# Optimization experiments

Hardware: AMD Instinct MI355X
Metric: run time of the kernel (lower is better)

Reference implementation:

```python
import jax, jax.numpy as jnp
import numpy as np

H = 1024; W = 1024
SPACE_SIGMA = 16.0; RANGE_SIGMA = 0.25
PAD_XY = 2; PAD_Z = 2
DIM = 5


def setup_inputs() -> dict:
    key = jax.random.key(0)
    k1, k2 = jax.random.split(key)
    features = jax.random.uniform(k1, (H, W, 3), dtype=jnp.float32)
    inp = jax.random.normal(k2, (H, W, 3), dtype=jnp.float32)
    return {"features": features, "inp": inp}


def _grid_dims(features_np):
    # Grid sizes are data-dependent in the original (TF builds them from
    # per-channel min/max); compute them host-side from concrete inputs.
    sh = int(float(H - 1) / SPACE_SIGMA) + 1 + 2 * PAD_XY
    sw = int(float(W - 1) / SPACE_SIGMA) + 1 + 2 * PAD_XY
    depths = []
    for c in range(3):
        ch = features_np[..., c]
        delta = float(ch.max() - ch.min())
        depths.append(int(delta / RANGE_SIGMA) + 1 + 2 * PAD_Z)
    return (sh, sw, depths[0], depths[1], depths[2])


def _both_indices(size, coord):
    left = jnp.clip(coord.astype(jnp.int32), 0, size - 1)
    right = jnp.clip(left + 1, 0, size - 1)
    return left, right


def _convn(data, n_iter=2):
    # Faithful port of the TF convn: separable [1,2,1]/4 pass per axis with
    # the exact same ping-pong buffer / boundary-keep / transpose behavior.
    buffer = jnp.zeros_like(data)
    perm = (1, 2, 3, 4, 0)
    for _ in range(n_iter):
        buffer, data = data, buffer
        for _ in range(DIM):
            newdata = (buffer[:-2] + buffer[2:] + 2.0 * buffer[1:-1]) / 4.0
            data = jnp.concatenate([data[:1], newdata, data[-1:]], axis=0)
            data = jnp.transpose(data, perm)
            buffer = jnp.transpose(buffer, perm)
    return data


def _filter(features, inp, dims):
    sh, sw, dr, dg, db = dims
    hw = H * W
    yy, xx = jnp.meshgrid(jnp.arange(H, dtype=jnp.float32),
                          jnp.arange(W, dtype=jnp.float32), indexing="ij")
    splat_yy = (yy / SPACE_SIGMA + 0.5).astype(jnp.int32) + PAD_XY
    splat_xx = (xx / SPACE_SIGMA + 0.5).astype(jnp.int32) + PAD_XY
    slice_yy = yy / SPACE_SIGMA + PAD_XY
    slice_xx = xx / SPACE_SIGMA + PAD_XY
    y_i, y_i2 = _both_indices(sh, slice_yy)
    x_i, x_i2 = _both_indices(sw, slice_xx)
    y_alpha = (slice_yy - y_i.astype(jnp.float32)).reshape(-1)
    x_alpha = (slice_xx - x_i.astype(jnp.float32)).reshape(-1)

    chans = []
    for c, depth in zip(range(3), (dr, dg, db)):
        v = features[..., c]
        v0 = v - jnp.min(v)
        splat_v = (v0 / RANGE_SIGMA + 0.5).astype(jnp.int32) + PAD_Z
        slice_v = v0 / RANGE_SIGMA + PAD_Z
        li, ri = _both_indices(depth, slice_v)
        alpha = (slice_v - li.astype(jnp.float32)).reshape(-1)
        chans.append((splat_v, li, ri, alpha))
    (splat_rr, r_i, r_i2, r_alpha) = chans[0]
    (splat_gg, g_i, g_i2, g_alpha) = chans[1]
    (splat_bb, b_i, b_i2, b_alpha) = chans[2]

    splat_coords = ((((splat_yy * sw + splat_xx) * dr + splat_rr) * dg
                     + splat_gg) * db + splat_bb).reshape(-1)  # [hw]

    idx_all = jnp.stack([y_i, y_i2, x_i, x_i2, r_i, r_i2,
                         g_i, g_i2, b_i, b_i2]).reshape(10, hw)
    alphas_all = jnp.stack([1.0 - y_alpha, y_alpha, 1.0 - x_alpha, x_alpha,
                            1.0 - r_alpha, r_alpha, 1.0 - g_alpha, g_alpha,
                            1.0 - b_alpha, b_alpha])  # [10, hw]

    # 32 corners of the 5-D hypercube; sel[c, d] picks left/right index per dim.
    corners = np.stack(np.meshgrid(*([np.arange(2)] * DIM), indexing="ij"),
                       axis=-1).reshape(-1, DIM)
    sel = corners + np.arange(DIM) * 2  # [32, 5]

    strides = (sw, dr, dg, db)
    coord = idx_all[sel[:, 0]]  # [32, hw]
    for d in range(1, DIM):
        coord = coord * strides[d - 1] + idx_all[sel[:, d]]
    alpha_prod = alphas_all[sel[:, 0]]  # [32, hw]
    for d in range(1, DIM):
        alpha_prod = alpha_prod * alphas_all[sel[:, d]]

    total = sh * sw * dr * dg * db

    def ch_filter(ch):
        grid = jnp.zeros((total,), jnp.float32).at[splat_coords].add(ch.reshape(-1))
        grid = _convn(grid.reshape(sh, sw, dr, dg, db))
        vals = grid.reshape(-1)[coord]  # [32, hw] multilinear gather
        return jnp.sum(alpha_prod * vals, axis=0).reshape(H, W)

    outT = jax.vmap(ch_filter)(jnp.transpose(inp, (2, 0, 1)))
    return jnp.transpose(outT, (1, 2, 0))


def reference(features, inp):
    dims = _grid_dims(np.asarray(features))
    return _filter(features, inp, dims)
```

## Files before the change

kernel.cpp:

```cpp
#include <hip/hip_runtime.h>

namespace {

constexpr int kH  = 1024;
constexpr int kW  = 1024;
constexpr int kHW = kH * kW;
constexpr int kSH = 68;
constexpr int kSW = 68;
constexpr int kD  = 8;
constexpr int kT3 = kSH * kSW * kD * kD * kD;

__global__ void minmax_kernel(const float* __restrict__ feat, float* __restrict__ part) {
    const float4* f4 = (const float4*)feat;
    float mn[3] = {1e30f, 1e30f, 1e30f};
    float mx[3] = {-1e30f, -1e30f, -1e30f};
    int tid = blockIdx.x * blockDim.x + threadIdx.x;
    int stride = gridDim.x * blockDim.x;
    for (int c = tid; c < kHW / 4; c += stride) {
        float4 q0 = f4[c * 3], q1 = f4[c * 3 + 1], q2 = f4[c * 3 + 2];
        mn[0] = fminf(mn[0], fminf(fminf(q0.x, q0.w), fminf(q1.z, q2.y)));
        mx[0] = fmaxf(mx[0], fmaxf(fmaxf(q0.x, q0.w), fmaxf(q1.z, q2.y)));
        mn[1] = fminf(mn[1], fminf(fminf(q0.y, q1.x), fminf(q1.w, q2.z)));
        mx[1] = fmaxf(mx[1], fmaxf(fmaxf(q0.y, q1.x), fmaxf(q1.w, q2.z)));
        mn[2] = fminf(mn[2], fminf(fminf(q0.z, q1.y), fminf(q2.x, q2.w)));
        mx[2] = fmaxf(mx[2], fmaxf(fmaxf(q0.z, q1.y), fmaxf(q2.x, q2.w)));
    }
    #pragma unroll
    for (int off = 32; off > 0; off >>= 1) {
        #pragma unroll
        for (int c = 0; c < 3; ++c) {
            mn[c] = fminf(mn[c], __shfl_down(mn[c], off, 64));
            mx[c] = fmaxf(mx[c], __shfl_down(mx[c], off, 64));
        }
    }
    __shared__ float smn[4][3], smx[4][3];
    int wave = threadIdx.x >> 6;
    if ((threadIdx.x & 63) == 0) {
        #pragma unroll
        for (int c = 0; c < 3; ++c) { smn[wave][c] = mn[c]; smx[wave][c] = mx[c]; }
    }
    __syncthreads();
    if (threadIdx.x == 0) {
        #pragma unroll
        for (int c = 0; c < 3; ++c) {
            part[blockIdx.x * 6 + c]     = fminf(fminf(smn[0][c], smn[1][c]), fminf(smn[2][c], smn[3][c]));
            part[blockIdx.x * 6 + 3 + c] = fmaxf(fmaxf(smx[0][c], smx[1][c]), fmaxf(smx[2][c], smx[3][c]));
        }
    }
}

__global__ void params_kernel(const float* __restrict__ part, float* __restrict__ hdrF) {
    int t = threadIdx.x;
    float mn[3], mx[3];
    #pragma unroll
    for (int c = 0; c < 3; ++c) { mn[c] = part[t * 6 + c]; mx[c] = part[t * 6 + 3 + c]; }
    #pragma unroll
    for (int off = 32; off > 0; off >>= 1) {
        #pragma unroll
        for (int c = 0; c < 3; ++c) {
            mn[c] = fminf(mn[c], __shfl_down(mn[c], off, 64));
            mx[c] = fmaxf(mx[c], __shfl_down(mx[c], off, 64));
        }
    }
    __shared__ float smn[4][3], smx[4][3];
    int wave = t >> 6;
    if ((t & 63) == 0) {
        #pragma unroll
        for (int c = 0; c < 3; ++c) { smn[wave][c] = mn[c]; smx[wave][c] = mx[c]; }
    }
    __syncthreads();
    if (t == 0) {
        int* ip = (int*)(hdrF + 8);
        #pragma unroll
        for (int c = 0; c < 3; ++c) {
            float bmn = fminf(fminf(smn[0][c], smn[1][c]), fminf(smn[2][c], smn[3][c]));
            float bmx = fmaxf(fmaxf(smx[0][c], smx[1][c]), fmaxf(smx[2][c], smx[3][c]));
            float delta = bmx - bmn;
            int depth = (int)((double)delta / 0.25) + 1 + 4;
            if (depth > kD) depth = kD;
            if (depth < 1) depth = 1;
            hdrF[c] = bmn;
            ip[c] = depth;
        }
    }
}

__global__ __launch_bounds__(256) void splat_kernel(const float* __restrict__ feat,
                                                    const float* __restrict__ inp,
                                                    const float* __restrict__ hdrF,
                                                    float* __restrict__ grid) {
    int ix = blockIdx.x, iy = blockIdx.y;
    int y0 = (iy == 0) ? 0 : 16 * iy - 8;
    int x0 = (ix == 0) ? 0 : 16 * ix - 8;
    int h = (iy == 0 || iy == 64) ? 8 : 16;
    int w = (ix == 0 || ix == 64) ? 8 : 16;

    __shared__ float acc[3 * 512];
    __shared__ float fS[16 * 48], iS[16 * 48];
    for (int i = threadIdx.x; i < 3 * 512; i += 256) acc[i] = 0.0f;

    int rowVec = (w * 3) >> 2;
    int nvec = h * rowVec;
    const float4* f4 = (const float4*)(feat + ((long)y0 * kW + x0) * 3);
    const float4* i4 = (const float4*)(inp  + ((long)y0 * kW + x0) * 3);
    for (int t = threadIdx.x; t < nvec; t += 256) {
        int row = t / rowVec, q = t - row * rowVec;
        ((float4*)fS)[row * rowVec + q] = f4[row * (kW * 3 / 4) + q];
        ((float4*)iS)[row * rowVec + q] = i4[row * (kW * 3 / 4) + q];
    }
    __syncthreads();

    int t = threadIdx.x;
    int n = w * h;
    if (t < n) {
        int lx = t & (w - 1);
        int ly = (w == 16) ? (t >> 4) : (t >> 3);
        int o = (ly * w + lx) * 3;
        float v0 = fS[o + 0] - hdrF[0];
        float v1 = fS[o + 1] - hdrF[1];
        float v2 = fS[o + 2] - hdrF[2];
        int sr = (int)(v0 * 4.0f + 0.5f) + 2;
        int sg = (int)(v1 * 4.0f + 0.5f) + 2;
        int sb = (int)(v2 * 4.0f + 0.5f) + 2;
        int ci = (sr << 6) + (sg << 3) + sb;
        atomicAdd(&acc[ci],        iS[o + 0]);
        atomicAdd(&acc[512 + ci],  iS[o + 1]);
        atomicAdd(&acc[1024 + ci], iS[o + 2]);
    }
    __syncthreads();

    long base = ((long)((iy + 2) * kSW + (ix + 2))) << 9;
    for (int i = threadIdx.x; i < 512; i += 256) {
        int b = i >> 6, r = (i >> 3) & 7, g = i & 7;
        int s = (r << 6) + (g << 3) + b;
        grid[base + i]            = acc[s];
        grid[kT3 + base + i]      = acc[512 + s];
        grid[2 * kT3 + base + i]  = acc[1024 + s];
    }
}

__global__ __launch_bounds__(192) void blur2_kernel(float* __restrict__ dst,
                                                    const float* __restrict__ src,
                                                    const float* __restrict__ hdrF) {
    int cx = blockIdx.x + 2, cy = blockIdx.y + 2;
    const int* ip = (const int*)(hdrF + 8);
    int dr = ip[0], dg = ip[1], db = ip[2];

    __shared__ float Sv[3 * 576];
    long cbase = ((long)(cy * kSW + cx)) << 9;

    {
        const float4* g4 = (const float4*)src;
        for (int i = threadIdx.x; i < 384; i += 192) {
            int ch = i >> 7, i4 = i & 127;
            float4 q = g4[(long)ch * (kT3 / 4) + (cbase >> 2) + i4];
            int b = i4 >> 4;
            int rg = ((i4 >> 1) & 7) * 8 + (i4 & 1) * 4;
            *(float4*)&Sv[ch * 576 + b * 72 + rg] = q;
        }
    }
    __syncthreads();

    int ch = threadIdx.x >> 6;
    int rg = threadIdx.x & 63;
    int r = rg >> 3, g = rg & 7;

    float* S = Sv + ch * 576;
    auto SV = [&](int b, int l) -> float { return S[b * 72 + l]; };
    auto gsp = [&](int ccy, int ccx, int rr, int gg, int bb) -> float {
        if (ccy < 2 || ccy > 66 || ccx < 2 || ccx > 66) return 0.0f;
        return src[(long)ch * kT3 + (((long)(ccy * kSW + ccx)) << 9) + (bb << 6) + (rr << 3) + gg];
    };

    bool gI = (g >= 1) && (g <= dg - 2);
    bool rI = (r >= 1) && (r <= dr - 2);

    float v[8];
    #pragma unroll
    for (int b = 0; b < 8; ++b) v[b] = SV(b, rg);

    int eHi = db - 1;

    auto o1_end = [&](int e) -> float {
        float Vm, Vp;
        if (gI)      { Vm = SV(e, rg - 1); Vp = SV(e, rg + 1); }
        else if (rI) { Vm = SV(e, rg - 8); Vp = SV(e, rg + 8); }
        else         { Vm = gsp(cy, cx - 1, r, g, e); Vp = gsp(cy, cx + 1, r, g, e); }
        return (Vm + Vp + 2.0f * SV(e, rg)) * 0.25f;
    };
    float o1_lo = o1_end(0);
    float o1_hi = o1_end(eHi);

    float o1[8];
    #pragma unroll
    for (int b = 0; b < 8; ++b) {
        float iv = 0.0f;
        if (b >= 1 && b <= 6) iv = ((v[b - 1] + v[b + 1]) + 2.0f * v[b]) * 0.25f;
        o1[b] = (b >= 1 && b <= db - 2) ? iv : (b == 0 ? o1_lo : (b == eHi ? o1_hi : 0.0f));
    }

    auto out1_in = [&](int r2, int g2, int e) -> float {
        int l2 = (r2 << 3) + g2;
        float C = SV(e, l2);
        float Nm, Np;
        if (g2 >= 1 && g2 <= dg - 2)      { Nm = SV(e, l2 - 1); Np = SV(e, l2 + 1); }
        else if (r2 >= 1 && r2 <= dr - 2) { Nm = SV(e, l2 - 8); Np = SV(e, l2 + 8); }
        else { Nm = gsp(cy, cx - 1, r2, g2, e); Np = gsp(cy, cx + 1, r2, g2, e); }
        return (Nm + Np + 2.0f * C) * 0.25f;
    };
    auto out1_x = [&](int cx2, int e) -> float {
        float C = gsp(cy, cx2, r, g, e);
        float Nm, Np;
        if (cx2 >= 1 && cx2 <= kSW - 2) { Nm = gsp(cy, cx2 - 1, r, g, e); Np = gsp(cy, cx2 + 1, r, g, e); }
        else                            { Nm = gsp(cy - 1, cx2, r, g, e); Np = gsp(cy + 1, cx2, r, g, e); }
        return (Nm + Np + 2.0f * C) * 0.25f;
    };
    auto o2_end = [&](int e, float o1e) -> float {
        float Xm, Xp;
        if (gI)      { Xm = out1_in(r, g - 1, e); Xp = out1_in(r, g + 1, e); }
        else if (rI) { Xm = out1_in(r - 1, g, e); Xp = out1_in(r + 1, g, e); }
        else         { Xm = out1_x(cx - 1, e);    Xp = out1_x(cx + 1, e); }
        return (Xm + Xp + 2.0f * o1e) * 0.25f;
    };
    float o2_lo = o2_end(0, o1_lo);
    float o2_hi = o2_end(eHi, o1_hi);

    float o2[8];
    #pragma unroll
    for (int b = 0; b < 8; ++b) {
        float iv = 0.0f;
        if (b >= 1 && b <= 6) iv = ((o1[b - 1] + o1[b + 1]) + 2.0f * o1[b]) * 0.25f;
        o2[b] = (b >= 1 && b <= db - 2) ? iv : (b == 0 ? o2_lo : (b == eHi ? o2_hi : 0.0f));
    }

    float* dp = dst + (long)ch * kT3 + cbase + (rg << 3);
    *(float4*)dp       = make_float4(o2[0], o2[1], o2[2], o2[3]);
    *(float4*)(dp + 4) = make_float4(o2[4], o2[5], o2[6], o2[7]);
}

__global__ __launch_bounds__(256) void slice_kernel(const float* __restrict__ feat,
                                                    const float* __restrict__ hdrF,
                                                    const float* __restrict__ grid,
                                                    float* __restrict__ out) {
    __shared__ float sg[3 * 4 * 512 + 8];
    int tx = blockIdx.x, ty = blockIdx.y;

    {
        const float4* g4 = (const float4*)grid;
        float4* s4 = (float4*)sg;
        #pragma unroll
        for (int it = 0; it < 2; ++it) {
            int i = threadIdx.x + it * 256;
            int cell = i >> 7;
            int ci4 = i & 127;
            int cy = ty + 2 + (cell >> 1), cx = tx + 2 + (cell & 1);
            long cbase4 = ((long)(cy * kSW + cx)) << 7;
            #pragma unroll
            for (int ch = 0; ch < 3; ++ch)
                s4[ch * 512 + i] = g4[(long)ch * (kT3 / 4) + cbase4 + ci4];
        }
    }
    __syncthreads();

    const int* ip = (const int*)(hdrF + 8);
    int d3[3] = {ip[0], ip[1], ip[2]};
    int lx = threadIdx.x & 15, ly = threadIdx.x >> 4;
    int y = (ty << 4) + ly, x = (tx << 4) + lx;
    int p = (y << 10) + x;

    float ya = (float)ly * 0.0625f;
    float xa = (float)lx * 0.0625f;

    int li[3], ri[3];
    float al[3];
    #pragma unroll
    for (int c = 0; c < 3; ++c) {
        float v0 = feat[p * 3 + c] - hdrF[c];
        float sv = v0 * 4.0f + 2.0f;
        int l = (int)sv;
        int dm = d3[c] - 1;
        l = l < 0 ? 0 : (l > dm ? dm : l);
        int rr = l + 1 > dm ? dm : l + 1;
        li[c] = l; ri[c] = rr; al[c] = sv - (float)l;
    }

    float spw[4];
    {
        float wy[2] = {1.0f - ya, ya};
        float wx[2] = {1.0f - xa, xa};
        spw[0] = wy[0] * wx[0]; spw[1] = wy[0] * wx[1];
        spw[2] = wy[1] * wx[0]; spw[3] = wy[1] * wx[1];
    }
    int rs[2] = {li[0], ri[0]}; float wrr[2] = {1.0f - al[0], al[0]};
    int gs[2] = {li[1], ri[1]}; float wgg[2] = {1.0f - al[1], al[1]};
    int bq = li[2];
    float aeff = (ri[2] > li[2]) ? al[2] : 0.0f;

    float acc0 = 0.0f, acc1 = 0.0f, acc2 = 0.0f;
    #pragma unroll
    for (int k = 0; k < 4; ++k) {
        #pragma unroll
        for (int cr = 0; cr < 2; ++cr)
        #pragma unroll
        for (int cg = 0; cg < 2; ++cg) {
            int si = (k << 9) + (rs[cr] << 6) + (gs[cg] << 3) + bq;
            float w = spw[k] * wrr[cr] * wgg[cg];
            float a0 = sg[si],        a1 = sg[si + 1];
            float b0 = sg[2048 + si], b1 = sg[2048 + si + 1];
            float c0 = sg[4096 + si], c1 = sg[4096 + si + 1];
            acc0 += w * (a0 + aeff * (a1 - a0));
            acc1 += w * (b0 + aeff * (b1 - b0));
            acc2 += w * (c0 + aeff * (c1 - c0));
        }
    }
    out[p * 3 + 0] = acc0;
    out[p * 3 + 1] = acc1;
    out[p * 3 + 2] = acc2;
}

}

extern "C" void kernel_launch(void* const* d_in, const int* in_sizes, int n_in,
                              void* d_out, int out_size, void* d_ws, size_t ws_size,
                              hipStream_t stream) {
    const float* feat = (const float*)d_in[0];
    const float* inp  = (const float*)d_in[1];
    float* out = (float*)d_out;

    float* hdrF  = (float*)d_ws;
    float* part  = (float*)((char*)d_ws + 1024);
    float* gridA = (float*)((char*)d_ws + 8192);
    float* gridB = gridA + 3 * (size_t)kT3;

    minmax_kernel<<<256, 256, 0, stream>>>(feat, part);
    params_kernel<<<1, 256, 0, stream>>>(part, hdrF);

    splat_kernel<<<dim3(65, 65), 256, 0, stream>>>(feat, inp, hdrF, gridA);
    blur2_kernel<<<dim3(65, 65), 192, 0, stream>>>(gridB, gridA, hdrF);
    slice_kernel<<<dim3(64, 64), 256, 0, stream>>>(feat, hdrF, gridB, out);
}
```

Before: 142.2 us.

## Fuse all stages into one persistent cooperative kernel with grid syncs

Replaces the five separate launches (minmax, params, splat, blur, slice) with a single cooperative kernel of 512 persistent blocks that loops over cells and tiles, separating the stages with grid.sync(). The aim is to remove per-launch overhead and the gaps between kernels. In exchange, each stage runs with only 512 blocks instead of thousands, and the grid-wide barriers add cost. The original kernels are kept as a fallback if the cooperative launch fails.

```diff
diff --git a/kernel.cpp b/kernel.cpp
--- a/kernel.cpp
+++ b/kernel.cpp
@@ -1,19 +1,348 @@
 #include <hip/hip_runtime.h>
+#include <hip/hip_cooperative_groups.h>
+
+namespace cg = cooperative_groups;
+
+#define kH  1024
+#define kW  1024
+#define kHW (kH * kW)
+#define kSH 68
+#define kSW 68
+#define kD  8
+#define kT3 (kSH * kSW * kD * kD * kD)
+#define kNB 512
 
 namespace {
 
-constexpr int kH  = 1024;
-constexpr int kW  = 1024;
-constexpr int kHW = kH * kW;
-constexpr int kSH = 68;
-constexpr int kSW = 68;
-constexpr int kD  = 8;
-constexpr int kT3 = kSH * kSW * kD * kD * kD;
-
-__global__ void minmax_kernel(const float* __restrict__ feat, float* __restrict__ part) {
+__global__ __launch_bounds__(256, 2)
+void mega_kernel(const float* __restrict__ feat,
+                 const float* __restrict__ inp,
+                 float* __restrict__ out,
+                 float* __restrict__ hdrF,
+                 float* __restrict__ part,
+                 float* __restrict__ gridA,
+                 float* __restrict__ gridB) {
+    cg::grid_group grid = cg::this_grid();
+    __shared__ float S[6160];
+
+    {
+        const float4* f4 = (const float4*)feat;
+        float mn[3] = {1e30f, 1e30f, 1e30f}, mx[3] = {-1e30f, -1e30f, -1e30f};
+        for (int c = blockIdx.x * 256 + threadIdx.x; c < kHW / 4; c += kNB * 256) {
+            float4 q0 = f4[c * 3], q1 = f4[c * 3 + 1], q2 = f4[c * 3 + 2];
+            mn[0] = fminf(mn[0], fminf(fminf(q0.x, q0.w), fminf(q1.z, q2.y)));
+            mx[0] = fmaxf(mx[0], fmaxf(fmaxf(q0.x, q0.w), fmaxf(q1.z, q2.y)));
+            mn[1] = fminf(mn[1], fminf(fminf(q0.y, q1.x), fminf(q1.w, q2.z)));
+            mx[1] = fmaxf(mx[1], fmaxf(fmaxf(q0.y, q1.x), fmaxf(q1.w, q2.z)));
+            mn[2] = fminf(mn[2], fminf(fminf(q0.z, q1.y), fminf(q2.x, q2.w)));
+            mx[2] = fmaxf(mx[2], fmaxf(fmaxf(q0.z, q1.y), fmaxf(q2.x, q2.w)));
+        }
+        #pragma unroll
+        for (int off = 32; off > 0; off >>= 1) {
+            #pragma unroll
+            for (int k = 0; k < 3; ++k) {
+                mn[k] = fminf(mn[k], __shfl_down(mn[k], off, 64));
+                mx[k] = fmaxf(mx[k], __shfl_down(mx[k], off, 64));
+            }
+        }
+        int wave = threadIdx.x >> 6;
+        if ((threadIdx.x & 63) == 0) {
+            #pragma unroll
+            for (int k = 0; k < 3; ++k) { S[wave * 3 + k] = mn[k]; S[12 + wave * 3 + k] = mx[k]; }
+        }
+        __syncthreads();
+        if (threadIdx.x == 0) {
+            #pragma unroll
+            for (int k = 0; k < 3; ++k) {
+                part[blockIdx.x * 6 + k]     = fminf(fminf(S[k], S[3 + k]), fminf(S[6 + k], S[9 + k]));
+                part[blockIdx.x * 6 + 3 + k] = fmaxf(fmaxf(S[12 + k], S[15 + k]), fmaxf(S[18 + k], S[21 + k]));
+            }
+        }
+        __syncthreads();
+    }
+    grid.sync();
+
+    if (blockIdx.x == 0) {
+        int t = threadIdx.x;
+        float mn[3] = {1e30f, 1e30f, 1e30f}, mx[3] = {-1e30f, -1e30f, -1e30f};
+        #pragma unroll
+        for (int j = 0; j < 2; ++j) {
+            int idx = t + j * 256;
+            #pragma unroll
+            for (int k = 0; k < 3; ++k) {
+                mn[k] = fminf(mn[k], part[idx * 6 + k]);
+                mx[k] = fmaxf(mx[k], part[idx * 6 + 3 + k]);
+            }
+        }
+        #pragma unroll
+        for (int off = 32; off > 0; off >>= 1) {
+            #pragma unroll
+            for (int k = 0; k < 3; ++k) {
+                mn[k] = fminf(mn[k], __shfl_down(mn[k], off, 64));
+                mx[k] = fmaxf(mx[k], __shfl_down(mx[k], off, 64));
+            }
+        }
+        int wave = t >> 6;
+        if ((t & 63) == 0) {
+            #pragma unroll
+            for (int k = 0; k < 3; ++k) { S[wave * 3 + k] = mn[k]; S[12 + wave * 3 + k] = mx[k]; }
+        }
+        __syncthreads();
+        if (t == 0) {
+            int* ip = (int*)(hdrF + 8);
+            #pragma unroll
+            for (int k = 0; k < 3; ++k) {
+                float bmn = fminf(fminf(S[k], S[3 + k]), fminf(S[6 + k], S[9 + k]));
+                float bmx = fmaxf(fmaxf(S[12 + k], S[15 + k]), fmaxf(S[18 + k], S[21 + k]));
+                float delta = bmx - bmn;
+                int depth = (int)((double)delta / 0.25) + 1 + 4;
+                if (depth > kD) depth = kD;
+                if (depth < 1) depth = 1;
+                hdrF[k] = bmn;
+                ip[k] = depth;
+            }
+        }
+    }
+    grid.sync();
+
+    float m0 = hdrF[0], m1 = hdrF[1], m2 = hdrF[2];
+    const int* ip = (const int*)(hdrF + 8);
+    int dr = ip[0], dg = ip[1], db = ip[2];
+
+    {
+        float* acc = S;
+        float* fS  = S + 1536;
+        float* iS  = S + 2304;
+        for (int cell = blockIdx.x; cell < 65 * 65; cell += kNB) {
+            int iy = cell / 65, ix = cell % 65;
+            int y0 = (iy == 0) ? 0 : 16 * iy - 8;
+            int x0 = (ix == 0) ? 0 : 16 * ix - 8;
+            int h = (iy == 0 || iy == 64) ? 8 : 16;
+            int w = (ix == 0 || ix == 64) ? 8 : 16;
+
+            for (int i = threadIdx.x; i < 1536; i += 256) acc[i] = 0.0f;
+
+            int rowVec = (w * 3) >> 2;
+            int nvec = h * rowVec;
+            const float4* f4 = (const float4*)(feat + ((long)y0 * kW + x0) * 3);
+            const float4* i4 = (const float4*)(inp  + ((long)y0 * kW + x0) * 3);
+            for (int t = threadIdx.x; t < nvec; t += 256) {
+                int row = t / rowVec, q = t - row * rowVec;
+                ((float4*)fS)[row * rowVec + q] = f4[row * (kW * 3 / 4) + q];
+                ((float4*)iS)[row * rowVec + q] = i4[row * (kW * 3 / 4) + q];
+            }
+            __syncthreads();
+
+            int t = threadIdx.x;
+            if (t < w * h) {
+                int lx = t & (w - 1);
+                int ly = (w == 16) ? (t >> 4) : (t >> 3);
+                int o = (ly * w + lx) * 3;
+                int sr  = (int)((fS[o + 0] - m0) * 4.0f + 0.5f) + 2;
+                int sg2 = (int)((fS[o + 1] - m1) * 4.0f + 0.5f) + 2;
+                int sb  = (int)((fS[o + 2] - m2) * 4.0f + 0.5f) + 2;
+                int ci = (sr << 6) + (sg2 << 3) + sb;
+                atomicAdd(&acc[ci],        iS[o + 0]);
+                atomicAdd(&acc[512 + ci],  iS[o + 1]);
+                atomicAdd(&acc[1024 + ci], iS[o + 2]);
+            }
+            __syncthreads();
+
+            long base = ((long)((iy + 2) * kSW + (ix + 2))) << 9;
+            for (int i = threadIdx.x; i < 512; i += 256) {
+                int b = i >> 6, r = (i >> 3) & 7, g = i & 7;
+                int s = (r << 6) + (g << 3) + b;
+                gridA[base + i]            = acc[s];
+                gridA[kT3 + base + i]      = acc[512 + s];
+                gridA[2 * kT3 + base + i]  = acc[1024 + s];
+            }
+            __syncthreads();
+        }
+    }
+    grid.sync();
+
+    {
+        float* Sv = S;
+        for (int cell = blockIdx.x; cell < 65 * 65; cell += kNB) {
+            int cy = cell / 65 + 2, cx = cell % 65 + 2;
+            long cbase = ((long)(cy * kSW + cx)) << 9;
+            {
+                const float4* g4 = (const float4*)gridA;
+                for (int i = threadIdx.x; i < 384; i += 256) {
+                    int ch = i >> 7, i4 = i & 127;
+                    float4 q = g4[(long)ch * (kT3 / 4) + (cbase >> 2) + i4];
+                    int b = i4 >> 4;
+                    int rg = ((i4 >> 1) & 7) * 8 + (i4 & 1) * 4;
+                    *(float4*)&Sv[ch * 576 + b * 72 + rg] = q;
+                }
+            }
+            __syncthreads();
+
+            if (threadIdx.x < 192) {
+                int ch = threadIdx.x >> 6;
+                int rg = threadIdx.x & 63;
+                int r = rg >> 3, g = rg & 7;
+
+                float* Sc = Sv + ch * 576;
+                auto SV = [&](int b, int l) -> float { return Sc[b * 72 + l]; };
+                auto gsp = [&](int ccy, int ccx, int rr, int gg, int bb) -> float {
+                    if (ccy < 2 || ccy > 66 || ccx < 2 || ccx > 66) return 0.0f;
+                    return gridA[(long)ch * kT3 + (((long)(ccy * kSW + ccx)) << 9) + (bb << 6) + (rr << 3) + gg];
+                };
+
+                bool gI = (g >= 1) && (g <= dg - 2);
+                bool rI = (r >= 1) && (r <= dr - 2);
+
+                float v[8];
+                #pragma unroll
+                for (int b = 0; b < 8; ++b) v[b] = SV(b, rg);
+
+                int eHi = db - 1;
+
+                auto o1_end = [&](int e) -> float {
+                    float Vm, Vp;
+                    if (gI)      { Vm = SV(e, rg - 1); Vp = SV(e, rg + 1); }
+                    else if (rI) { Vm = SV(e, rg - 8); Vp = SV(e, rg + 8); }
+                    else         { Vm = gsp(cy, cx - 1, r, g, e); Vp = gsp(cy, cx + 1, r, g, e); }
+                    return (Vm + Vp + 2.0f * SV(e, rg)) * 0.25f;
+                };
+                float o1_lo = o1_end(0);
+                float o1_hi = o1_end(eHi);
+
+                float o1[8];
+                #pragma unroll
+                for (int b = 0; b < 8; ++b) {
+                    float iv = 0.0f;
+                    if (b >= 1 && b <= 6) iv = ((v[b - 1] + v[b + 1]) + 2.0f * v[b]) * 0.25f;
+                    o1[b] = (b >= 1 && b <= db - 2) ? iv : (b == 0 ? o1_lo : (b == eHi ? o1_hi : 0.0f));
+                }
+
+                auto out1_in = [&](int r2, int g2, int e) -> float {
+                    int l2 = (r2 << 3) + g2;
+                    float C = SV(e, l2);
+                    float Nm, Np;
+                    if (g2 >= 1 && g2 <= dg - 2)      { Nm = SV(e, l2 - 1); Np = SV(e, l2 + 1); }
+                    else if (r2 >= 1 && r2 <= dr - 2) { Nm = SV(e, l2 - 8); Np = SV(e, l2 + 8); }
+                    else { Nm = gsp(cy, cx - 1, r2, g2, e); Np = gsp(cy, cx + 1, r2, g2, e); }
+                    return (Nm + Np + 2.0f * C) * 0.25f;
+                };
+                auto out1_x = [&](int cx2, int e) -> float {
+                    float C = gsp(cy, cx2, r, g, e);
+                    float Nm, Np;
+                    if (cx2 >= 1 && cx2 <= kSW - 2) { Nm = gsp(cy, cx2 - 1, r, g, e); Np = gsp(cy, cx2 + 1, r, g, e); }
+                    else                            { Nm = gsp(cy - 1, cx2, r, g, e); Np = gsp(cy + 1, cx2, r, g, e); }
+                    return (Nm + Np + 2.0f * C) * 0.25f;
+                };
+                auto o2_end = [&](int e, float o1e) -> float {
+                    float Xm, Xp;
+                    if (gI)      { Xm = out1_in(r, g - 1, e); Xp = out1_in(r, g + 1, e); }
+                    else if (rI) { Xm = out1_in(r - 1, g, e); Xp = out1_in(r + 1, g, e); }
+                    else         { Xm = out1_x(cx - 1, e);    Xp = out1_x(cx + 1, e); }
+                    return (Xm + Xp + 2.0f * o1e) * 0.25f;
+                };
+                float o2_lo = o2_end(0, o1_lo);
+                float o2_hi = o2_end(eHi, o1_hi);
+
+                float o2[8];
+                #pragma unroll
+                for (int b = 0; b < 8; ++b) {
+                    float iv = 0.0f;
+                    if (b >= 1 && b <= 6) iv = ((o1[b - 1] + o1[b + 1]) + 2.0f * o1[b]) * 0.25f;
+                    o2[b] = (b >= 1 && b <= db - 2) ? iv : (b == 0 ? o2_lo : (b == eHi ? o2_hi : 0.0f));
+                }
+
+                float* dp = gridB + (long)ch * kT3 + cbase + (rg << 3);
+                *(float4*)dp       = make_float4(o2[0], o2[1], o2[2], o2[3]);
+                *(float4*)(dp + 4) = make_float4(o2[4], o2[5], o2[6], o2[7]);
+            }
+            __syncthreads();
+        }
+    }
+    grid.sync();
+
+    {
+        float* sg = S;
+        for (int tile = blockIdx.x; tile < 64 * 64; tile += kNB) {
+            int ty = tile >> 6, tx = tile & 63;
+            {
+                const float4* g4 = (const float4*)gridB;
+                float4* s4 = (float4*)sg;
+                #pragma unroll
+                for (int it = 0; it < 2; ++it) {
+                    int i = threadIdx.x + it * 256;
+                    int cell = i >> 7;
+                    int ci4 = i & 127;
+                    int cy = ty + 2 + (cell >> 1), cx = tx + 2 + (cell & 1);
+                    long cbase4 = ((long)(cy * kSW + cx)) << 7;
+                    #pragma unroll
+                    for (int ch = 0; ch < 3; ++ch)
+                        s4[ch * 512 + i] = g4[(long)ch * (kT3 / 4) + cbase4 + ci4];
+                }
+            }
+            __syncthreads();
+
+            int lx = threadIdx.x & 15, ly = threadIdx.x >> 4;
+            int y = (ty << 4) + ly, x = (tx << 4) + lx;
+            int p = (y << 10) + x;
+
+            float ya = (float)ly * 0.0625f;
+            float xa = (float)lx * 0.0625f;
+
+            int d3[3] = {dr, dg, db};
+            float mm[3] = {m0, m1, m2};
+            int li[3], ri[3];
+            float al[3];
+            #pragma unroll
+            for (int c = 0; c < 3; ++c) {
+                float v0 = feat[p * 3 + c] - mm[c];
+                float sv = v0 * 4.0f + 2.0f;
+                int l = (int)sv;
+                int dm = d3[c] - 1;
+                l = l < 0 ? 0 : (l > dm ? dm : l);
+                int rr = l + 1 > dm ? dm : l + 1;
+                li[c] = l; ri[c] = rr; al[c] = sv - (float)l;
+            }
+
+            float spw[4];
+            {
+                float wy[2] = {1.0f - ya, ya};
+                float wx[2] = {1.0f - xa, xa};
+                spw[0] = wy[0] * wx[0]; spw[1] = wy[0] * wx[1];
+                spw[2] = wy[1] * wx[0]; spw[3] = wy[1] * wx[1];
+            }
+            int rs[2] = {li[0], ri[0]}; float wrr[2] = {1.0f - al[0], al[0]};
+            int gs[2] = {li[1], ri[1]}; float wgg[2] = {1.0f - al[1], al[1]};
+            int bq = li[2];
+            float aeff = (ri[2] > li[2]) ? al[2] : 0.0f;
+
+            float acc0 = 0.0f, acc1 = 0.0f, acc2 = 0.0f;
+            #pragma unroll
+            for (int k = 0; k < 4; ++k) {
+                #pragma unroll
+                for (int cr = 0; cr < 2; ++cr)
+                #pragma unroll
+                for (int cg = 0; cg < 2; ++cg) {
+                    int si = (k << 9) + (rs[cr] << 6) + (gs[cg] << 3) + bq;
+                    float w = spw[k] * wrr[cr] * wgg[cg];
+                    float a0 = sg[si],        a1 = sg[si + 1];
+                    float b0 = sg[2048 + si], b1 = sg[2048 + si + 1];
+                    float c0 = sg[4096 + si], c1 = sg[4096 + si + 1];
+                    acc0 += w * (a0 + aeff * (a1 - a0));
+                    acc1 += w * (b0 + aeff * (b1 - b0));
+                    acc2 += w * (c0 + aeff * (c1 - c0));
+                }
+            }
+            out[p * 3 + 0] = acc0;
+            out[p * 3 + 1] = acc1;
+            out[p * 3 + 2] = acc2;
+            __syncthreads();
+        }
+    }
+}
+
+__global__ void fb_minmax(const float* __restrict__ feat, float* __restrict__ part) {
     const float4* f4 = (const float4*)feat;
-    float mn[3] = {1e30f, 1e30f, 1e30f};
-    float mx[3] = {-1e30f, -1e30f, -1e30f};
+    float mn[3] = {1e30f, 1e30f, 1e30f}, mx[3] = {-1e30f, -1e30f, -1e30f};
     int tid = blockIdx.x * blockDim.x + threadIdx.x;
     int stride = gridDim.x * blockDim.x;
     for (int c = tid; c < kHW / 4; c += stride) {
@@ -49,7 +378,7 @@
     }
 }
 
-__global__ void params_kernel(const float* __restrict__ part, float* __restrict__ hdrF) {
+__global__ void fb_params(const float* __restrict__ part, float* __restrict__ hdrF) {
     int t = threadIdx.x;
     float mn[3], mx[3];
     #pragma unroll
@@ -85,10 +414,10 @@
     }
 }
 
-__global__ __launch_bounds__(256) void splat_kernel(const float* __restrict__ feat,
-                                                    const float* __restrict__ inp,
-                                                    const float* __restrict__ hdrF,
-                                                    float* __restrict__ grid) {
+__global__ __launch_bounds__(256) void fb_splat(const float* __restrict__ feat,
+                                                const float* __restrict__ inp,
+                                                const float* __restrict__ hdrF,
+                                                float* __restrict__ grid) {
     int ix = blockIdx.x, iy = blockIdx.y;
     int y0 = (iy == 0) ? 0 : 16 * iy - 8;
     int x0 = (ix == 0) ? 0 : 16 * ix - 8;
@@ -111,17 +440,13 @@
     __syncthreads();
 
     int t = threadIdx.x;
-    int n = w * h;
-    if (t < n) {
+    if (t < w * h) {
         int lx = t & (w - 1);
         int ly = (w == 16) ? (t >> 4) : (t >> 3);
         int o = (ly * w + lx) * 3;
-        float v0 = fS[o + 0] - hdrF[0];
-        float v1 = fS[o + 1] - hdrF[1];
-        float v2 = fS[o + 2] - hdrF[2];
-        int sr = (int)(v0 * 4.0f + 0.5f) + 2;
-        int sg = (int)(v1 * 4.0f + 0.5f) + 2;
-        int sb = (int)(v2 * 4.0f + 0.5f) + 2;
+        int sr = (int)((fS[o + 0] - hdrF[0]) * 4.0f + 0.5f) + 2;
+        int sg = (int)((fS[o + 1] - hdrF[1]) * 4.0f + 0.5f) + 2;
+        int sb = (int)((fS[o + 2] - hdrF[2]) * 4.0f + 0.5f) + 2;
         int ci = (sr << 6) + (sg << 3) + sb;
         atomicAdd(&acc[ci],        iS[o + 0]);
         atomicAdd(&acc[512 + ci],  iS[o + 1]);
@@ -139,9 +464,9 @@
     }
 }
 
-__global__ __launch_bounds__(192) void blur2_kernel(float* __restrict__ dst,
-                                                    const float* __restrict__ src,
-                                                    const float* __restrict__ hdrF) {
+__global__ __launch_bounds__(192) void fb_blur2(float* __restrict__ dst,
+                                                const float* __restrict__ src,
+                                                const float* __restrict__ hdrF) {
     int cx = blockIdx.x + 2, cy = blockIdx.y + 2;
     const int* ip = (const int*)(hdrF + 8);
     int dr = ip[0], dg = ip[1], db = ip[2];
@@ -238,10 +563,10 @@
     *(float4*)(dp + 4) = make_float4(o2[4], o2[5], o2[6], o2[7]);
 }
 
-__global__ __launch_bounds__(256) void slice_kernel(const float* __restrict__ feat,
-                                                    const float* __restrict__ hdrF,
-                                                    const float* __restrict__ grid,
-                                                    float* __restrict__ out) {
+__global__ __launch_bounds__(256) void fb_slice(const float* __restrict__ feat,
+                                                const float* __restrict__ hdrF,
+                                                const float* __restrict__ grid,
+                                                float* __restrict__ out) {
     __shared__ float sg[3 * 4 * 512 + 8];
     int tx = blockIdx.x, ty = blockIdx.y;
 
@@ -328,14 +653,19 @@
     float* out = (float*)d_out;
 
     float* hdrF  = (float*)d_ws;
-    float* part  = (float*)((char*)d_ws + 1024);
-    float* gridA = (float*)((char*)d_ws + 8192);
+    float* part  = (float*)((char*)d_ws + 16384);
+    float* gridA = (float*)((char*)d_ws + 65536);
     float* gridB = gridA + 3 * (size_t)kT3;
 
-    minmax_kernel<<<256, 256, 0, stream>>>(feat, part);
-    params_kernel<<<1, 256, 0, stream>>>(part, hdrF);
-
-    splat_kernel<<<dim3(65, 65), 256, 0, stream>>>(feat, inp, hdrF, gridA);
-    blur2_kernel<<<dim3(65, 65), 192, 0, stream>>>(gridB, gridA, hdrF);
-    slice_kernel<<<dim3(64, 64), 256, 0, stream>>>(feat, hdrF, gridB, out);
-}
+    void* args[] = {(void*)&feat, (void*)&inp, (void*)&out,
+                    (void*)&hdrF, (void*)&part, (void*)&gridA, (void*)&gridB};
+    hipError_t err = hipLaunchCooperativeKernel((const void*)mega_kernel, dim3(kNB),
+                                                dim3(256), args, 0, stream);
+    if (err != hipSuccess) {
+        fb_minmax<<<256, 256, 0, stream>>>(feat, part);
+        fb_params<<<1, 256, 0, stream>>>(part, hdrF);
+        fb_splat<<<dim3(65, 65), 256, 0, stream>>>(feat, inp, hdrF, gridA);
+        fb_blur2<<<dim3(65, 65), 192, 0, stream>>>(gridB, gridA, hdrF);
+        fb_slice<<<dim3(64, 64), 256, 0, stream>>>(feat, hdrF, gridB, out);
+    }
+}
```

Measured after the change: 386.3 us. 2.72x slower.

## Store bilateral grids in fp16 and fold the params reduction into consumer kernels

Applied to the files above, without the earlier changes.

The intermediate splat and blurred grids are now stored as half precision, halving their memory footprint and traffic in splat, blur and slice, with conversion to float on load into shared memory. The single-block params kernel is removed. Each consumer block instead re-reduces the 256 per-block min/max partials itself, which drops one launch and its serialization but repeats a small reduction in every block. fp16 storage of accumulated grid sums adds rounding error and could overflow for large sums.

```diff
diff --git a/kernel.cpp b/kernel.cpp
--- a/kernel.cpp
+++ b/kernel.cpp
@@ -1,4 +1,5 @@
 #include <hip/hip_runtime.h>
+#include <hip/hip_fp16.h>
 
 namespace {
 
@@ -10,10 +11,51 @@
 constexpr int kD  = 8;
 constexpr int kT3 = kSH * kSW * kD * kD * kD;
 
+template <int NT>
+__device__ inline void load_params(const float* __restrict__ part,
+                                   float mOut[3], int dOut[3]) {
+    __shared__ float pm[NT / 64][6];
+    float mn[3] = {1e30f, 1e30f, 1e30f}, mx[3] = {-1e30f, -1e30f, -1e30f};
+    for (int idx = threadIdx.x; idx < 256; idx += NT) {
+        #pragma unroll
+        for (int c = 0; c < 3; ++c) {
+            mn[c] = fminf(mn[c], part[idx * 6 + c]);
+            mx[c] = fmaxf(mx[c], part[idx * 6 + 3 + c]);
+        }
+    }
+    #pragma unroll
+    for (int off = 32; off > 0; off >>= 1) {
+        #pragma unroll
+        for (int c = 0; c < 3; ++c) {
+            mn[c] = fminf(mn[c], __shfl_down(mn[c], off, 64));
+            mx[c] = fmaxf(mx[c], __shfl_down(mx[c], off, 64));
+        }
+    }
+    int wave = threadIdx.x >> 6;
+    if ((threadIdx.x & 63) == 0) {
+        #pragma unroll
+        for (int c = 0; c < 3; ++c) { pm[wave][c] = mn[c]; pm[wave][3 + c] = mx[c]; }
+    }
+    __syncthreads();
+    #pragma unroll
+    for (int c = 0; c < 3; ++c) {
+        float bmn = pm[0][c], bmx = pm[0][3 + c];
+        #pragma unroll
+        for (int w = 1; w < NT / 64; ++w) {
+            bmn = fminf(bmn, pm[w][c]);
+            bmx = fmaxf(bmx, pm[w][3 + c]);
+        }
+        float delta = bmx - bmn;
+        int depth = (int)((double)delta / 0.25) + 1 + 4;
+        depth = depth > kD ? kD : (depth < 1 ? 1 : depth);
+        mOut[c] = bmn;
+        dOut[c] = depth;
+    }
+}
+
 __global__ void minmax_kernel(const float* __restrict__ feat, float* __restrict__ part) {
     const float4* f4 = (const float4*)feat;
-    float mn[3] = {1e30f, 1e30f, 1e30f};
-    float mx[3] = {-1e30f, -1e30f, -1e30f};
+    float mn[3] = {1e30f, 1e30f, 1e30f}, mx[3] = {-1e30f, -1e30f, -1e30f};
     int tid = blockIdx.x * blockDim.x + threadIdx.x;
     int stride = gridDim.x * blockDim.x;
     for (int c = tid; c < kHW / 4; c += stride) {
@@ -49,46 +91,13 @@
     }
 }
 
-__global__ void params_kernel(const float* __restrict__ part, float* __restrict__ hdrF) {
-    int t = threadIdx.x;
-    float mn[3], mx[3];
-    #pragma unroll
-    for (int c = 0; c < 3; ++c) { mn[c] = part[t * 6 + c]; mx[c] = part[t * 6 + 3 + c]; }
-    #pragma unroll
-    for (int off = 32; off > 0; off >>= 1) {
-        #pragma unroll
-        for (int c = 0; c < 3; ++c) {
-            mn[c] = fminf(mn[c], __shfl_down(mn[c], off, 64));
-            mx[c] = fmaxf(mx[c], __shfl_down(mx[c], off, 64));
-        }
-    }
-    __shared__ float smn[4][3], smx[4][3];
-    int wave = t >> 6;
-    if ((t & 63) == 0) {
-        #pragma unroll
-        for (int c = 0; c < 3; ++c) { smn[wave][c] = mn[c]; smx[wave][c] = mx[c]; }
-    }
-    __syncthreads();
-    if (t == 0) {
-        int* ip = (int*)(hdrF + 8);
-        #pragma unroll
-        for (int c = 0; c < 3; ++c) {
-            float bmn = fminf(fminf(smn[0][c], smn[1][c]), fminf(smn[2][c], smn[3][c]));
-            float bmx = fmaxf(fmaxf(smx[0][c], smx[1][c]), fmaxf(smx[2][c], smx[3][c]));
-            float delta = bmx - bmn;
-            int depth = (int)((double)delta / 0.25) + 1 + 4;
-            if (depth > kD) depth = kD;
-            if (depth < 1) depth = 1;
-            hdrF[c] = bmn;
-            ip[c] = depth;
-        }
-    }
-}
-
 __global__ __launch_bounds__(256) void splat_kernel(const float* __restrict__ feat,
                                                     const float* __restrict__ inp,
-                                                    const float* __restrict__ hdrF,
-                                                    float* __restrict__ grid) {
+                                                    const float* __restrict__ part,
+                                                    __half* __restrict__ grid) {
+    float mm[3]; int dd[3];
+    load_params<256>(part, mm, dd);
+
     int ix = blockIdx.x, iy = blockIdx.y;
     int y0 = (iy == 0) ? 0 : 16 * iy - 8;
     int x0 = (ix == 0) ? 0 : 16 * ix - 8;
@@ -111,17 +120,13 @@
     __syncthreads();
 
     int t = threadIdx.x;
-    int n = w * h;
-    if (t < n) {
+    if (t < w * h) {
         int lx = t & (w - 1);
         int ly = (w == 16) ? (t >> 4) : (t >> 3);
         int o = (ly * w + lx) * 3;
-        float v0 = fS[o + 0] - hdrF[0];
-        float v1 = fS[o + 1] - hdrF[1];
-        float v2 = fS[o + 2] - hdrF[2];
-        int sr = (int)(v0 * 4.0f + 0.5f) + 2;
-        int sg = (int)(v1 * 4.0f + 0.5f) + 2;
-        int sb = (int)(v2 * 4.0f + 0.5f) + 2;
+        int sr = (int)((fS[o + 0] - mm[0]) * 4.0f + 0.5f) + 2;
+        int sg = (int)((fS[o + 1] - mm[1]) * 4.0f + 0.5f) + 2;
+        int sb = (int)((fS[o + 2] - mm[2]) * 4.0f + 0.5f) + 2;
         int ci = (sr << 6) + (sg << 3) + sb;
         atomicAdd(&acc[ci],        iS[o + 0]);
         atomicAdd(&acc[512 + ci],  iS[o + 1]);
@@ -130,33 +135,39 @@
     __syncthreads();
 
     long base = ((long)((iy + 2) * kSW + (ix + 2))) << 9;
-    for (int i = threadIdx.x; i < 512; i += 256) {
-        int b = i >> 6, r = (i >> 3) & 7, g = i & 7;
-        int s = (r << 6) + (g << 3) + b;
-        grid[base + i]            = acc[s];
-        grid[kT3 + base + i]      = acc[512 + s];
-        grid[2 * kT3 + base + i]  = acc[1024 + s];
-    }
-}
-
-__global__ __launch_bounds__(192) void blur2_kernel(float* __restrict__ dst,
-                                                    const float* __restrict__ src,
-                                                    const float* __restrict__ hdrF) {
+    for (int i = threadIdx.x; i < 768; i += 256) {
+        int ch = i >> 8, p = i & 255;
+        int g = (2 * p) & 7, r = ((2 * p) >> 3) & 7, b = (2 * p) >> 6;
+        int s0 = (r << 6) + (g << 3) + b;
+        __half2 hv = __halves2half2(__float2half_rn(acc[ch * 512 + s0]),
+                                    __float2half_rn(acc[ch * 512 + s0 + 8]));
+        ((__half2*)(grid + (long)ch * kT3 + base))[p] = hv;
+    }
+}
+
+__global__ __launch_bounds__(192) void blur2_kernel(__half* __restrict__ dst,
+                                                    const __half* __restrict__ src,
+                                                    const float* __restrict__ part) {
+    float mm[3]; int dd[3];
+    load_params<192>(part, mm, dd);
+    int dr = dd[0], dg = dd[1], db = dd[2];
+
     int cx = blockIdx.x + 2, cy = blockIdx.y + 2;
-    const int* ip = (const int*)(hdrF + 8);
-    int dr = ip[0], dg = ip[1], db = ip[2];
-
     __shared__ float Sv[3 * 576];
     long cbase = ((long)(cy * kSW + cx)) << 9;
 
     {
-        const float4* g4 = (const float4*)src;
-        for (int i = threadIdx.x; i < 384; i += 192) {
-            int ch = i >> 7, i4 = i & 127;
-            float4 q = g4[(long)ch * (kT3 / 4) + (cbase >> 2) + i4];
-            int b = i4 >> 4;
-            int rg = ((i4 >> 1) & 7) * 8 + (i4 & 1) * 4;
-            *(float4*)&Sv[ch * 576 + b * 72 + rg] = q;
+        for (int i = threadIdx.x; i < 192; i += 192) {
+            int ch = i >> 6, i8 = i & 63;
+            float4 q = ((const float4*)(src + (long)ch * kT3 + cbase))[i8];
+            int b = i8 >> 3, r = i8 & 7;
+            float2 f0 = __half22float2(*(__half2*)&q.x);
+            float2 f1 = __half22float2(*((__half2*)&q.x + 1));
+            float2 f2 = __half22float2(*(__half2*)&q.z);
+            float2 f3 = __half22float2(*((__half2*)&q.z + 1));
+            float* S = Sv + ch * 576 + b * 72 + r * 8;
+            S[0] = f0.x; S[1] = f0.y; S[2] = f1.x; S[3] = f1.y;
+            S[4] = f2.x; S[5] = f2.y; S[6] = f3.x; S[7] = f3.y;
         }
     }
     __syncthreads();
@@ -169,7 +180,8 @@
     auto SV = [&](int b, int l) -> float { return S[b * 72 + l]; };
     auto gsp = [&](int ccy, int ccx, int rr, int gg, int bb) -> float {
         if (ccy < 2 || ccy > 66 || ccx < 2 || ccx > 66) return 0.0f;
-        return src[(long)ch * kT3 + (((long)(ccy * kSW + ccx)) << 9) + (bb << 6) + (rr << 3) + gg];
+        return __half2float(src[(long)ch * kT3 + (((long)(ccy * kSW + ccx)) << 9) +
+                                (bb << 6) + (rr << 3) + gg]);
     };
 
     bool gI = (g >= 1) && (g <= dg - 2);
@@ -233,37 +245,46 @@
         o2[b] = (b >= 1 && b <= db - 2) ? iv : (b == 0 ? o2_lo : (b == eHi ? o2_hi : 0.0f));
     }
 
-    float* dp = dst + (long)ch * kT3 + cbase + (rg << 3);
-    *(float4*)dp       = make_float4(o2[0], o2[1], o2[2], o2[3]);
-    *(float4*)(dp + 4) = make_float4(o2[4], o2[5], o2[6], o2[7]);
+    __half2 h0 = __halves2half2(__float2half_rn(o2[0]), __float2half_rn(o2[1]));
+    __half2 h1 = __halves2half2(__float2half_rn(o2[2]), __float2half_rn(o2[3]));
+    __half2 h2 = __halves2half2(__float2half_rn(o2[4]), __float2half_rn(o2[5]));
+    __half2 h3 = __halves2half2(__float2half_rn(o2[6]), __float2half_rn(o2[7]));
+    float4 pack;
+    *(__half2*)&pack.x = h0; *((__half2*)&pack.x + 1) = h1;
+    *(__half2*)&pack.z = h2; *((__half2*)&pack.z + 1) = h3;
+    ((float4*)(dst + (long)ch * kT3 + cbase))[rg] = pack;
 }
 
 __global__ __launch_bounds__(256) void slice_kernel(const float* __restrict__ feat,
-                                                    const float* __restrict__ hdrF,
-                                                    const float* __restrict__ grid,
+                                                    const float* __restrict__ part,
+                                                    const __half* __restrict__ gridB,
                                                     float* __restrict__ out) {
+    float mm[3]; int dd[3];
+    load_params<256>(part, mm, dd);
+
     __shared__ float sg[3 * 4 * 512 + 8];
     int tx = blockIdx.x, ty = blockIdx.y;
 
     {
-        const float4* g4 = (const float4*)grid;
-        float4* s4 = (float4*)sg;
-        #pragma unroll
-        for (int it = 0; it < 2; ++it) {
-            int i = threadIdx.x + it * 256;
-            int cell = i >> 7;
-            int ci4 = i & 127;
+        for (int j = 0; j < 3; ++j) {
+            int id = threadIdx.x + j * 256;
+            int cell = id / 192;
+            int rem = id - cell * 192;
+            int ch = rem >> 6, line = rem & 63;
             int cy = ty + 2 + (cell >> 1), cx = tx + 2 + (cell & 1);
-            long cbase4 = ((long)(cy * kSW + cx)) << 7;
-            #pragma unroll
-            for (int ch = 0; ch < 3; ++ch)
-                s4[ch * 512 + i] = g4[(long)ch * (kT3 / 4) + cbase4 + ci4];
-        }
-    }
-    __syncthreads();
-
-    const int* ip = (const int*)(hdrF + 8);
-    int d3[3] = {ip[0], ip[1], ip[2]};
+            float4 q = ((const float4*)(gridB + (long)ch * kT3 +
+                                        (((long)(cy * kSW + cx)) << 9)))[line];
+            float2 f0 = __half22float2(*(__half2*)&q.x);
+            float2 f1 = __half22float2(*((__half2*)&q.x + 1));
+            float2 f2 = __half22float2(*(__half2*)&q.z);
+            float2 f3 = __half22float2(*((__half2*)&q.z + 1));
+            float* d = sg + ch * 2048 + cell * 512 + line * 8;
+            ((float4*)d)[0] = make_float4(f0.x, f0.y, f1.x, f1.y);
+            ((float4*)d)[1] = make_float4(f2.x, f2.y, f3.x, f3.y);
+        }
+    }
+    __syncthreads();
+
     int lx = threadIdx.x & 15, ly = threadIdx.x >> 4;
     int y = (ty << 4) + ly, x = (tx << 4) + lx;
     int p = (y << 10) + x;
@@ -275,10 +296,10 @@
     float al[3];
     #pragma unroll
     for (int c = 0; c < 3; ++c) {
-        float v0 = feat[p * 3 + c] - hdrF[c];
+        float v0 = feat[p * 3 + c] - mm[c];
         float sv = v0 * 4.0f + 2.0f;
         int l = (int)sv;
-        int dm = d3[c] - 1;
+        int dm = dd[c] - 1;
         l = l < 0 ? 0 : (l > dm ? dm : l);
         int rr = l + 1 > dm ? dm : l + 1;
         li[c] = l; ri[c] = rr; al[c] = sv - (float)l;
@@ -327,15 +348,12 @@
     const float* inp  = (const float*)d_in[1];
     float* out = (float*)d_out;
 
-    float* hdrF  = (float*)d_ws;
-    float* part  = (float*)((char*)d_ws + 1024);
-    float* gridA = (float*)((char*)d_ws + 8192);
-    float* gridB = gridA + 3 * (size_t)kT3;
+    float*  part  = (float*)((char*)d_ws + 1024);
+    __half* gridA = (__half*)((char*)d_ws + 65536);
+    __half* gridB = gridA + 3 * (size_t)kT3;
 
     minmax_kernel<<<256, 256, 0, stream>>>(feat, part);
-    params_kernel<<<1, 256, 0, stream>>>(part, hdrF);
-
-    splat_kernel<<<dim3(65, 65), 256, 0, stream>>>(feat, inp, hdrF, gridA);
-    blur2_kernel<<<dim3(65, 65), 192, 0, stream>>>(gridB, gridA, hdrF);
-    slice_kernel<<<dim3(64, 64), 256, 0, stream>>>(feat, hdrF, gridB, out);
-}
+    splat_kernel<<<dim3(65, 65), 256, 0, stream>>>(feat, inp, part, gridA);
+    blur2_kernel<<<dim3(65, 65), 192, 0, stream>>>(gridB, gridA, part);
+    slice_kernel<<<dim3(64, 64), 256, 0, stream>>>(feat, part, gridB, out);
+}
```

Result: slower. 163.6 us (+15.0%).
